# Performance work log

Hardware: AMD Instinct MI355X
Metric: run time of the kernel (lower is better)

Reference implementation:

```python
import jax, jax.numpy as jnp
import numpy as np

B, T, D, H = 16, 4096, 256, 512  # batch, seq_len, ninputs, nhiddens


def setup_inputs() -> dict:
    key = jax.random.key(0)
    k_x, k_ih, k_hh, k_b, k_bn = jax.random.split(key, 5)
    s = 1.0 / np.sqrt(H)
    xs = jax.random.normal(k_x, (B, T, D), dtype=jnp.float32)
    W_ih = jax.random.uniform(k_ih, (3 * H, D), minval=-s, maxval=s, dtype=jnp.float32)
    W_hh = jax.random.uniform(k_hh, (3 * H, H), minval=-s, maxval=s, dtype=jnp.float32)
    b = jax.random.uniform(k_b, (3 * H,), minval=-s, maxval=s, dtype=jnp.float32)
    b_n = jax.random.uniform(k_bn, (H,), minval=-s, maxval=s, dtype=jnp.float32)
    return {"xs": xs, "W_ih": W_ih, "W_hh": W_hh, "b": b, "b_n": b_n}


def _gru_scan(xs, W_ih, W_hh, b, b_n):
    # Precompute all input-side gates with one big GEMM: (B, T, 3H)
    igates = jnp.einsum('btd,gd->btg', xs, W_ih) + b

    def step(h, ig):
        # h: (B, H), ig: (B, 3H)
        hg = h @ W_hh.T  # (B, 3H)
        i_r, i_z, i_n = jnp.split(ig, 3, axis=-1)
        h_r, h_z, h_n = jnp.split(hg, 3, axis=-1)
        r = jax.nn.sigmoid(i_r + h_r)   # reset gate
        z = jax.nn.sigmoid(i_z + h_z)   # update gate (equinox 'inp')
        n = jnp.tanh(i_n + r * (h_n + b_n))
        h_new = n + z * (h - n)         # equinox: new + inp * (hidden - new)
        return h_new, h_new

    h0 = jnp.zeros((xs.shape[0], b_n.shape[0]), dtype=xs.dtype)
    _, ys = jax.lax.scan(step, h0, jnp.swapaxes(igates, 0, 1))  # (T, B, H)
    return jnp.swapaxes(ys, 0, 1)  # (B, T, H)


def reference(xs, W_ih, W_hh, b, b_n):
    # CellLayer('gru', 'deer') computes the exact GRU recurrence over time
    # (DEER's fixed point equals the sequential evaluation).
    return _gru_scan(xs, W_ih, W_hh, b, b_n)
```

## Files before the change

kernel.cpp:

```cpp
#include <hip/hip_runtime.h>
#include <stdint.h>
#include <stddef.h>

#define B_ 16
#define T_ 4096
#define D_ 256
#define H_ 512
#define G3_ 1536

#define OFF_IG   ((size_t)0)
#define OFF_WT   ((size_t)201326592)
#define OFF_MB   ((size_t)202899456)
#define WS_NEED  ((size_t)203423744)

#define PAR_STRIDE ((size_t)B_ * 8 * 512)

typedef _Float16 h2_t __attribute__((ext_vector_type(2)));

#if defined(__has_builtin)
#if __has_builtin(__builtin_amdgcn_fdot2)
#define HAVE_FDOT2 1
#endif
#endif

__device__ __forceinline__ float fdot2f(uint32_t w, uint32_t h, float acc) {
  union { uint32_t u; h2_t v; } a, b;
  a.u = w; b.u = h;
#ifdef HAVE_FDOT2
  return __builtin_amdgcn_fdot2(a.v, b.v, acc, false);
#else
  return fmaf((float)a.v.x, (float)b.v.x, fmaf((float)a.v.y, (float)b.v.y, acc));
#endif
}

__device__ __forceinline__ uint32_t packh2(float a, float b) {
  union { h2_t v; uint32_t u; } x;
  x.v.x = (_Float16)a; x.v.y = (_Float16)b;
  return x.u;
}

__device__ __forceinline__ uint32_t f16bits(float a) {
  union { _Float16 h; uint16_t u; } x;
  x.h = (_Float16)a;
  return (uint32_t)x.u;
}

__device__ __forceinline__ float h2f(uint16_t u) {
  union { _Float16 h; uint16_t u; } x;
  x.u = u;
  return (float)x.h;
}

__device__ __forceinline__ float sigmoidf_(float x) {
  return 1.0f / (1.0f + __expf(-x));
}

__device__ __forceinline__ float tanhf_(float x) {
  x = fminf(fmaxf(x, -15.0f), 15.0f);
  float e = __expf(-2.0f * x);
  return (1.0f - e) / (1.0f + e);
}

__global__ void __launch_bounds__(256) wt_kernel(const float* __restrict__ W, float4* __restrict__ Wt4) {
  int idx = blockIdx.x * 256 + threadIdx.x;
  if (idx >= G3_ * 64) return;
  int g = idx % G3_;
  int d4 = idx / G3_;
  float4 v = *(const float4*)(W + (size_t)g * D_ + 4 * d4);
  Wt4[(size_t)d4 * G3_ + g] = v;
}

__global__ void __launch_bounds__(256) ig_kernel(const float* __restrict__ xs,
                                                 const float* __restrict__ Wt,
                                                 const float* __restrict__ bias,
                                                 _Float16* __restrict__ ig) {
  __shared__ float xls[16 * 256];
  const int m0 = blockIdx.x * 16;
  const int tid = threadIdx.x;

  const float4* xsrc = (const float4*)(xs + (size_t)m0 * D_);
  float4* xdst = (float4*)xls;
#pragma unroll
  for (int k = 0; k < 4; ++k) xdst[tid + 256 * k] = xsrc[tid + 256 * k];
  __syncthreads();

  float acc[6][16];
#pragma unroll
  for (int k = 0; k < 6; ++k)
#pragma unroll
    for (int m = 0; m < 16; ++m) acc[k][m] = 0.0f;

  const float4* Wt4 = (const float4*)Wt;
  const float4* lds4 = (const float4*)xls;

  for (int d4 = 0; d4 < 64; ++d4) {
    float4 w[6];
#pragma unroll
    for (int k = 0; k < 6; ++k) w[k] = Wt4[(size_t)d4 * G3_ + tid + 256 * k];
#pragma unroll
    for (int m = 0; m < 16; ++m) {
      float4 xv = lds4[m * 64 + d4];
#pragma unroll
      for (int k = 0; k < 6; ++k) {
        acc[k][m] = fmaf(w[k].x, xv.x, acc[k][m]);
        acc[k][m] = fmaf(w[k].y, xv.y, acc[k][m]);
        acc[k][m] = fmaf(w[k].z, xv.z, acc[k][m]);
        acc[k][m] = fmaf(w[k].w, xv.w, acc[k][m]);
      }
    }
  }

#pragma unroll
  for (int k = 0; k < 6; ++k) {
    float bb = bias[tid + 256 * k];
#pragma unroll
    for (int m = 0; m < 16; ++m) {
      ig[(size_t)(m0 + m) * G3_ + tid + 256 * k] = (_Float16)(acc[k][m] + bb);
    }
  }
}

__global__ void __launch_bounds__(512, 1) rec_kernel(const _Float16* __restrict__ ig,
                                                     const float* __restrict__ Whh,
                                                     const float* __restrict__ bn,
                                                     uint32_t* __restrict__ mb,
                                                     float* __restrict__ out) {
  const int tid = threadIdx.x;
  const int wg = blockIdx.x;
  const int b = wg >> 3;
  const int s = wg & 7;
  const int q = tid & 7;
  const int c = tid >> 3;
  const int j = s * 64 + c;

  uint32_t wr[32], wz[32], wn[32];
  {
    const float4* s0 = (const float4*)(Whh + (size_t)j * H_ + q * 64);
    const float4* s1 = (const float4*)(Whh + (size_t)(j + H_) * H_ + q * 64);
    const float4* s2 = (const float4*)(Whh + (size_t)(j + 2 * H_) * H_ + q * 64);
#pragma unroll
    for (int i = 0; i < 16; ++i) {
      float4 v0 = s0[i]; wr[2 * i] = packh2(v0.x, v0.y); wr[2 * i + 1] = packh2(v0.z, v0.w);
      float4 v1 = s1[i]; wz[2 * i] = packh2(v1.x, v1.y); wz[2 * i + 1] = packh2(v1.z, v1.w);
      float4 v2 = s2[i]; wn[2 * i] = packh2(v2.x, v2.y); wn[2 * i + 1] = packh2(v2.z, v2.w);
    }
  }
  const float bnj = bn[j];

  __shared__ uint32_t hl[2][8][36];
  uint16_t* hl16 = (uint16_t*)hl;

  uint32_t* mypoll = mb + ((size_t)b * 8 + s) * 512 + tid;
  uint32_t* mypub  = mb + ((size_t)b * 8 + q) * 512 + j;

  const uint16_t* ig16 = (const uint16_t*)ig;
  size_t igbase = (size_t)b * T_ * G3_;

  uint16_t cr = ig16[igbase + j];
  uint16_t cz = ig16[igbase + j + H_];
  uint16_t cn = ig16[igbase + j + 2 * H_];
  uint16_t r1 = ig16[igbase + G3_ + j];
  uint16_t z1 = ig16[igbase + G3_ + j + H_];
  uint16_t n1 = ig16[igbase + G3_ + j + 2 * H_];
  uint16_t r2 = ig16[igbase + 2 * (size_t)G3_ + j];
  uint16_t z2 = ig16[igbase + 2 * (size_t)G3_ + j + H_];
  uint16_t n2 = ig16[igbase + 2 * (size_t)G3_ + j + 2 * H_];

  float hprev = 0.0f;

  for (int t = 0; t < T_; ++t) {
    uint16_t fr = 0, fz = 0, fn = 0;

    if (t > 0) {
      uint32_t* pb = mypoll + (size_t)(t & 1) * PAR_STRIDE;
      const uint32_t want = (uint32_t)t;
      uint32_t va, vb, a0 = 0;
      asm volatile("global_load_dword %0, %2, off sc1\n\t"
                   "global_load_dword %1, %2, off sc1"
                   : "=&v"(va), "=&v"(vb) : "v"(pb) : "memory");
      int it = 0;
      for (;;) {
        asm volatile("s_waitcnt vmcnt(1)" ::: "memory");
        __builtin_amdgcn_sched_barrier(0);
        a0 = va;
        if ((a0 >> 16) == want) break;
        asm volatile("global_load_dword %0, %1, off sc1" : "=&v"(va) : "v"(pb) : "memory");
        asm volatile("s_waitcnt vmcnt(1)" ::: "memory");
        __builtin_amdgcn_sched_barrier(0);
        a0 = vb;
        if ((a0 >> 16) == want) break;
        asm volatile("global_load_dword %0, %1, off sc1" : "=&v"(vb) : "v"(pb) : "memory");
        if (++it > (1 << 20)) { a0 = 0x7C00u; break; }
      }
      asm volatile("s_waitcnt vmcnt(0)" ::: "memory");
      __builtin_amdgcn_sched_barrier(0);

      hl16[(t & 1) * 576 + (tid >> 6) * 72 + (tid & 63)] = (uint16_t)(a0 & 0xFFFFu);
    }

    if (t + 3 < T_) {
      const size_t fb = igbase + 3 * (size_t)G3_;
      fr = ig16[fb + j];
      fz = ig16[fb + j + H_];
      fn = ig16[fb + j + 2 * H_];
    }

    __syncthreads();

    float ar = 0.0f, az = 0.0f, an = 0.0f;
    if (t > 0) {
      const uint4* hq = (const uint4*)hl[t & 1][q];
      uint4 hv[8];
#pragma unroll
      for (int i = 0; i < 8; ++i) hv[i] = hq[i];
      float ar0 = 0.0f, az0 = 0.0f, an0 = 0.0f;
      float ar1 = 0.0f, az1 = 0.0f, an1 = 0.0f;
#pragma unroll
      for (int i = 0; i < 4; ++i) {
        ar0 = fdot2f(wr[4 * i + 0], hv[i].x, ar0); az0 = fdot2f(wz[4 * i + 0], hv[i].x, az0); an0 = fdot2f(wn[4 * i + 0], hv[i].x, an0);
        ar0 = fdot2f(wr[4 * i + 1], hv[i].y, ar0); az0 = fdot2f(wz[4 * i + 1], hv[i].y, az0); an0 = fdot2f(wn[4 * i + 1], hv[i].y, an0);
        ar0 = fdot2f(wr[4 * i + 2], hv[i].z, ar0); az0 = fdot2f(wz[4 * i + 2], hv[i].z, az0); an0 = fdot2f(wn[4 * i + 2], hv[i].z, an0);
        ar0 = fdot2f(wr[4 * i + 3], hv[i].w, ar0); az0 = fdot2f(wz[4 * i + 3], hv[i].w, az0); an0 = fdot2f(wn[4 * i + 3], hv[i].w, an0);
      }
#pragma unroll
      for (int i = 4; i < 8; ++i) {
        ar1 = fdot2f(wr[4 * i + 0], hv[i].x, ar1); az1 = fdot2f(wz[4 * i + 0], hv[i].x, az1); an1 = fdot2f(wn[4 * i + 0], hv[i].x, an1);
        ar1 = fdot2f(wr[4 * i + 1], hv[i].y, ar1); az1 = fdot2f(wz[4 * i + 1], hv[i].y, az1); an1 = fdot2f(wn[4 * i + 1], hv[i].y, an1);
        ar1 = fdot2f(wr[4 * i + 2], hv[i].z, ar1); az1 = fdot2f(wz[4 * i + 2], hv[i].z, az1); an1 = fdot2f(wn[4 * i + 2], hv[i].z, an1);
        ar1 = fdot2f(wr[4 * i + 3], hv[i].w, ar1); az1 = fdot2f(wz[4 * i + 3], hv[i].w, az1); an1 = fdot2f(wn[4 * i + 3], hv[i].w, an1);
      }
      ar = ar0 + ar1; az = az0 + az1; an = an0 + an1;
      ar += __shfl_xor(ar, 1); ar += __shfl_xor(ar, 2); ar += __shfl_xor(ar, 4);
      az += __shfl_xor(az, 1); az += __shfl_xor(az, 2); az += __shfl_xor(az, 4);
      an += __shfl_xor(an, 1); an += __shfl_xor(an, 2); an += __shfl_xor(an, 4);
    }

    const float igr = h2f(cr), igz = h2f(cz), ign = h2f(cn);
    const float r = sigmoidf_(igr + ar);
    const float z = sigmoidf_(igz + az);
    const float n = tanhf_(ign + r * (an + bnj));
    const float hnew = n + z * (hprev - n);
    hprev = hnew;

    const uint32_t wv = ((uint32_t)(t + 1) << 16) | f16bits(hnew);
    __hip_atomic_store(mypub + (size_t)((t + 1) & 1) * PAR_STRIDE, wv,
                       __ATOMIC_RELAXED, __HIP_MEMORY_SCOPE_AGENT);
    if (q == 0) {
      out[((size_t)b * T_ + t) * H_ + j] = hnew;
    }
    asm volatile("s_waitcnt vmcnt(0)" ::: "memory");
    __builtin_amdgcn_sched_barrier(0);

    cr = r1; cz = z1; cn = n1;
    r1 = r2; z1 = z2; n1 = n2;
    r2 = fr; z2 = fz; n2 = fn;
    igbase += G3_;
  }
}

__global__ void __launch_bounds__(512) naive_kernel(const float* __restrict__ xs,
                                                    const float* __restrict__ Wih,
                                                    const float* __restrict__ Whh,
                                                    const float* __restrict__ bias,
                                                    const float* __restrict__ bn,
                                                    float* __restrict__ out) {
  const int b = blockIdx.x;
  const int j = threadIdx.x;
  __shared__ float h[H_];
  __shared__ float xr[D_];
  h[j] = 0.0f;
  __syncthreads();
  for (int t = 0; t < T_; ++t) {
    if (j < D_) xr[j] = xs[((size_t)b * T_ + t) * D_ + j];
    __syncthreads();
    float a[2];
#pragma unroll
    for (int g = 0; g < 2; ++g) {
      const int row = j + g * H_;
      float ssum = bias[row];
      const float* wi = Wih + (size_t)row * D_;
      for (int d = 0; d < D_; ++d) ssum = fmaf(wi[d], xr[d], ssum);
      const float* wh = Whh + (size_t)row * H_;
      for (int kk = 0; kk < H_; ++kk) ssum = fmaf(wh[kk], h[kk], ssum);
      a[g] = ssum;
    }
    const float r = sigmoidf_(a[0]);
    const float z = sigmoidf_(a[1]);
    float i_n = bias[j + 2 * H_];
    {
      const float* wi = Wih + (size_t)(j + 2 * H_) * D_;
      for (int d = 0; d < D_; ++d) i_n = fmaf(wi[d], xr[d], i_n);
    }
    float h_n = 0.0f;
    {
      const float* wh = Whh + (size_t)(j + 2 * H_) * H_;
      for (int kk = 0; kk < H_; ++kk) h_n = fmaf(wh[kk], h[kk], h_n);
    }
    const float nn = tanhf_(i_n + r * (h_n + bn[j]));
    const float hnew = nn + z * (h[j] - nn);
    __syncthreads();
    h[j] = hnew;
    out[((size_t)b * T_ + t) * H_ + j] = hnew;
  }
}

extern "C" void kernel_launch(void* const* d_in, const int* in_sizes, int n_in,
                              void* d_out, int out_size, void* d_ws, size_t ws_size,
                              hipStream_t stream) {
  const float* xs  = (const float*)d_in[0];
  const float* Wih = (const float*)d_in[1];
  const float* Whh = (const float*)d_in[2];
  const float* bia = (const float*)d_in[3];
  const float* bnp = (const float*)d_in[4];
  float* out = (float*)d_out;

  if (ws_size >= WS_NEED) {
    char* ws = (char*)d_ws;
    _Float16* igp = (_Float16*)(ws + OFF_IG);
    float* wtp = (float*)(ws + OFF_WT);
    uint32_t* mbp = (uint32_t*)(ws + OFF_MB);

    hipMemsetAsync(mbp, 0, 2 * PAR_STRIDE * sizeof(uint32_t), stream);

    wt_kernel<<<dim3(384), dim3(256), 0, stream>>>(Wih, (float4*)wtp);
    ig_kernel<<<dim3((B_ * T_) / 16), dim3(256), 0, stream>>>(xs, wtp, bia, igp);
    rec_kernel<<<dim3(128), dim3(512), 0, stream>>>(igp, Whh, bnp, mbp, out);
  } else {
    naive_kernel<<<dim3(B_), dim3(H_), 0, stream>>>(xs, Wih, Whh, bia, bnp, out);
  }
}
```

Baseline: 7.269 ms.

## Interleave mailbox by hidden unit so pollers read all slice copies in one vector load

The inter-block mailbox layout changes from [batch][slice][unit] to [batch][unit][slice], so the eight published copies of each hidden value sit in 32 contiguous bytes. Each poller now issues two dwordx4 loads covering all eight copies and accepts whichever carries the current step tag, instead of polling only its own slice's copy. The aim is to cut spin latency in the recurrent synchronization, since any publisher that arrives first satisfies the wait. In exchange, each poll moves more bytes, and the outstanding loads are left in flight until the step's final waitcnt.

```diff
diff --git a/kernel.cpp b/kernel.cpp
--- a/kernel.cpp
+++ b/kernel.cpp
@@ -13,7 +13,7 @@
 #define OFF_MB   ((size_t)202899456)
 #define WS_NEED  ((size_t)203423744)
 
-#define PAR_STRIDE ((size_t)B_ * 8 * 512)
+#define PAR_STRIDE ((size_t)B_ * 512 * 8)
 
 typedef _Float16 h2_t __attribute__((ext_vector_type(2)));
 
@@ -150,8 +150,8 @@
   __shared__ uint32_t hl[2][8][36];
   uint16_t* hl16 = (uint16_t*)hl;
 
-  uint32_t* mypoll = mb + ((size_t)b * 8 + s) * 512 + tid;
-  uint32_t* mypub  = mb + ((size_t)b * 8 + q) * 512 + j;
+  uint32_t* mypoll = mb + ((size_t)b * 512 + tid) * 8;
+  uint32_t* mypub  = mb + ((size_t)b * 512 + j) * 8 + q;
 
   const uint16_t* ig16 = (const uint16_t*)ig;
   size_t igbase = (size_t)b * T_ * G3_;
@@ -170,30 +170,35 @@
 
   for (int t = 0; t < T_; ++t) {
     uint16_t fr = 0, fz = 0, fn = 0;
+    uint4 xa = {0, 0, 0, 0}, xb = {0, 0, 0, 0};
 
     if (t > 0) {
       uint32_t* pb = mypoll + (size_t)(t & 1) * PAR_STRIDE;
       const uint32_t want = (uint32_t)t;
-      uint32_t va, vb, a0 = 0;
-      asm volatile("global_load_dword %0, %2, off sc1\n\t"
-                   "global_load_dword %1, %2, off sc1"
-                   : "=&v"(va), "=&v"(vb) : "v"(pb) : "memory");
+      uint32_t a0 = 0;
+      asm volatile("global_load_dwordx4 %0, %2, off sc1\n\t"
+                   "global_load_dwordx4 %1, %2, off offset:16 sc1"
+                   : "=&v"(xa), "=&v"(xb) : "v"(pb) : "memory");
       int it = 0;
       for (;;) {
         asm volatile("s_waitcnt vmcnt(1)" ::: "memory");
         __builtin_amdgcn_sched_barrier(0);
-        a0 = va;
-        if ((a0 >> 16) == want) break;
-        asm volatile("global_load_dword %0, %1, off sc1" : "=&v"(va) : "v"(pb) : "memory");
+        {
+          bool m0 = (xa.x >> 16) == want, m1 = (xa.y >> 16) == want;
+          bool m2 = (xa.z >> 16) == want, m3 = (xa.w >> 16) == want;
+          if (m0 | m1 | m2 | m3) { a0 = m0 ? xa.x : m1 ? xa.y : m2 ? xa.z : xa.w; break; }
+        }
+        asm volatile("global_load_dwordx4 %0, %1, off sc1" : "=&v"(xa) : "v"(pb) : "memory");
         asm volatile("s_waitcnt vmcnt(1)" ::: "memory");
         __builtin_amdgcn_sched_barrier(0);
-        a0 = vb;
-        if ((a0 >> 16) == want) break;
-        asm volatile("global_load_dword %0, %1, off sc1" : "=&v"(vb) : "v"(pb) : "memory");
+        {
+          bool m0 = (xb.x >> 16) == want, m1 = (xb.y >> 16) == want;
+          bool m2 = (xb.z >> 16) == want, m3 = (xb.w >> 16) == want;
+          if (m0 | m1 | m2 | m3) { a0 = m0 ? xb.x : m1 ? xb.y : m2 ? xb.z : xb.w; break; }
+        }
+        asm volatile("global_load_dwordx4 %0, %1, off offset:16 sc1" : "=&v"(xb) : "v"(pb) : "memory");
         if (++it > (1 << 20)) { a0 = 0x7C00u; break; }
       }
-      asm volatile("s_waitcnt vmcnt(0)" ::: "memory");
-      __builtin_amdgcn_sched_barrier(0);
 
       hl16[(t & 1) * 576 + (tid >> 6) * 72 + (tid & 63)] = (uint16_t)(a0 & 0xFFFFu);
     }
@@ -248,6 +253,8 @@
     if (q == 0) {
       out[((size_t)b * T_ + t) * H_ + j] = hnew;
     }
+    asm volatile("" :: "v"(xa.x), "v"(xa.y), "v"(xa.z), "v"(xa.w),
+                       "v"(xb.x), "v"(xb.y), "v"(xb.z), "v"(xb.w));
     asm volatile("s_waitcnt vmcnt(0)" ::: "memory");
     __builtin_amdgcn_sched_barrier(0);
 
@@ -320,7 +327,7 @@
     float* wtp = (float*)(ws + OFF_WT);
     uint32_t* mbp = (uint32_t*)(ws + OFF_MB);
 
-    hipMemsetAsync(mbp, 0, 2 * PAR_STRIDE * sizeof(uint32_t), stream);
+    (void)hipMemsetAsync(mbp, 0, 2 * PAR_STRIDE * sizeof(uint32_t), stream);
 
     wt_kernel<<<dim3(384), dim3(256), 0, stream>>>(Wih, (float4*)wtp);
     ig_kernel<<<dim3((B_ * T_) / 16), dim3(256), 0, stream>>>(xs, wtp, bia, igp);
```

After: 8.933 ms. 1.23x slower.

## Process two batch elements per recurrent workgroup, halving grid size

Applied to the files above, without the earlier changes.

Each recurrent workgroup now handles two batch rows (b and b+8) with the same register-resident W_hh slice, polling both mailboxes and computing both matvecs per step. The grid shrinks from 128 to 64 workgroups, so the cross-workgroup synchronization footprint shrinks and the loaded weights serve twice the work. The cost is a longer serial per-step critical path, since two polls and two matvecs run back-to-back inside each timestep.

```diff
diff --git a/kernel.cpp b/kernel.cpp
--- a/kernel.cpp
+++ b/kernel.cpp
@@ -127,7 +127,8 @@
                                                      float* __restrict__ out) {
   const int tid = threadIdx.x;
   const int wg = blockIdx.x;
-  const int b = wg >> 3;
+  const int b0 = wg >> 3;
+  const int b1 = b0 + 8;
   const int s = wg & 7;
   const int q = tid & 7;
   const int c = tid >> 3;
@@ -147,114 +148,179 @@
   }
   const float bnj = bn[j];
 
-  __shared__ uint32_t hl[2][8][36];
+  __shared__ uint32_t hl[2][2][8][36];
   uint16_t* hl16 = (uint16_t*)hl;
 
-  uint32_t* mypoll = mb + ((size_t)b * 8 + s) * 512 + tid;
-  uint32_t* mypub  = mb + ((size_t)b * 8 + q) * 512 + j;
+  uint32_t* poll0 = mb + ((size_t)b0 * 8 + s) * 512 + tid;
+  uint32_t* poll1 = mb + ((size_t)b1 * 8 + s) * 512 + tid;
+  uint32_t* pub0  = mb + ((size_t)b0 * 8 + q) * 512 + j;
+  uint32_t* pub1  = mb + ((size_t)b1 * 8 + q) * 512 + j;
 
   const uint16_t* ig16 = (const uint16_t*)ig;
-  size_t igbase = (size_t)b * T_ * G3_;
-
-  uint16_t cr = ig16[igbase + j];
-  uint16_t cz = ig16[igbase + j + H_];
-  uint16_t cn = ig16[igbase + j + 2 * H_];
-  uint16_t r1 = ig16[igbase + G3_ + j];
-  uint16_t z1 = ig16[igbase + G3_ + j + H_];
-  uint16_t n1 = ig16[igbase + G3_ + j + 2 * H_];
-  uint16_t r2 = ig16[igbase + 2 * (size_t)G3_ + j];
-  uint16_t z2 = ig16[igbase + 2 * (size_t)G3_ + j + H_];
-  uint16_t n2 = ig16[igbase + 2 * (size_t)G3_ + j + 2 * H_];
-
-  float hprev = 0.0f;
+  size_t igb0 = (size_t)b0 * T_ * G3_;
+  size_t igb1 = (size_t)b1 * T_ * G3_;
+
+  uint16_t cr0 = ig16[igb0 + j], cz0 = ig16[igb0 + j + H_], cn0 = ig16[igb0 + j + 2 * H_];
+  uint16_t r10 = ig16[igb0 + G3_ + j], z10 = ig16[igb0 + G3_ + j + H_], n10 = ig16[igb0 + G3_ + j + 2 * H_];
+  uint16_t r20 = ig16[igb0 + 2 * (size_t)G3_ + j], z20 = ig16[igb0 + 2 * (size_t)G3_ + j + H_], n20 = ig16[igb0 + 2 * (size_t)G3_ + j + 2 * H_];
+  uint16_t cr1 = ig16[igb1 + j], cz1 = ig16[igb1 + j + H_], cn1 = ig16[igb1 + j + 2 * H_];
+  uint16_t r11_ = ig16[igb1 + G3_ + j], z11 = ig16[igb1 + G3_ + j + H_], n11 = ig16[igb1 + G3_ + j + 2 * H_];
+  uint16_t r21 = ig16[igb1 + 2 * (size_t)G3_ + j], z21 = ig16[igb1 + 2 * (size_t)G3_ + j + H_], n21 = ig16[igb1 + 2 * (size_t)G3_ + j + 2 * H_];
+
+  float hprev0 = 0.0f, hprev1 = 0.0f;
 
   for (int t = 0; t < T_; ++t) {
-    uint16_t fr = 0, fz = 0, fn = 0;
+    uint16_t fr0 = 0, fz0 = 0, fn0 = 0, fr1 = 0, fz1 = 0, fn1 = 0;
 
     if (t > 0) {
-      uint32_t* pb = mypoll + (size_t)(t & 1) * PAR_STRIDE;
       const uint32_t want = (uint32_t)t;
-      uint32_t va, vb, a0 = 0;
-      asm volatile("global_load_dword %0, %2, off sc1\n\t"
-                   "global_load_dword %1, %2, off sc1"
-                   : "=&v"(va), "=&v"(vb) : "v"(pb) : "memory");
-      int it = 0;
-      for (;;) {
-        asm volatile("s_waitcnt vmcnt(1)" ::: "memory");
+      const size_t poff = (size_t)(t & 1) * PAR_STRIDE;
+
+      {
+        uint32_t* pb = poll0 + poff;
+        uint32_t va, vb, a0;
+        asm volatile("global_load_dword %0, %2, off sc1\n\t"
+                     "global_load_dword %1, %2, off sc1"
+                     : "=&v"(va), "=&v"(vb) : "v"(pb) : "memory");
+        int it = 0;
+        for (;;) {
+          asm volatile("s_waitcnt vmcnt(1)" ::: "memory");
+          __builtin_amdgcn_sched_barrier(0);
+          a0 = va;
+          if ((a0 >> 16) == want) break;
+          asm volatile("global_load_dword %0, %1, off sc1" : "=&v"(va) : "v"(pb) : "memory");
+          asm volatile("s_waitcnt vmcnt(1)" ::: "memory");
+          __builtin_amdgcn_sched_barrier(0);
+          a0 = vb;
+          if ((a0 >> 16) == want) break;
+          asm volatile("global_load_dword %0, %1, off sc1" : "=&v"(vb) : "v"(pb) : "memory");
+          if (++it > (1 << 20)) { a0 = 0x7C00u; break; }
+        }
+        asm volatile("s_waitcnt vmcnt(0)" :: "v"(va), "v"(vb) : "memory");
         __builtin_amdgcn_sched_barrier(0);
-        a0 = va;
-        if ((a0 >> 16) == want) break;
-        asm volatile("global_load_dword %0, %1, off sc1" : "=&v"(va) : "v"(pb) : "memory");
-        asm volatile("s_waitcnt vmcnt(1)" ::: "memory");
+        hl16[(t & 1) * 576 + (tid >> 6) * 72 + (tid & 63)] = (uint16_t)(a0 & 0xFFFFu);
+      }
+
+      {
+        uint32_t* pb = poll1 + poff;
+        uint32_t va, vb, a1;
+        asm volatile("global_load_dword %0, %2, off sc1\n\t"
+                     "global_load_dword %1, %2, off sc1"
+                     : "=&v"(va), "=&v"(vb) : "v"(pb) : "memory");
+        int it = 0;
+        for (;;) {
+          asm volatile("s_waitcnt vmcnt(1)" ::: "memory");
+          __builtin_amdgcn_sched_barrier(0);
+          a1 = va;
+          if ((a1 >> 16) == want) break;
+          asm volatile("global_load_dword %0, %1, off sc1" : "=&v"(va) : "v"(pb) : "memory");
+          asm volatile("s_waitcnt vmcnt(1)" ::: "memory");
+          __builtin_amdgcn_sched_barrier(0);
+          a1 = vb;
+          if ((a1 >> 16) == want) break;
+          asm volatile("global_load_dword %0, %1, off sc1" : "=&v"(vb) : "v"(pb) : "memory");
+          if (++it > (1 << 20)) { a1 = 0x7C00u; break; }
+        }
+        asm volatile("s_waitcnt vmcnt(0)" :: "v"(va), "v"(vb) : "memory");
         __builtin_amdgcn_sched_barrier(0);
-        a0 = vb;
-        if ((a0 >> 16) == want) break;
-        asm volatile("global_load_dword %0, %1, off sc1" : "=&v"(vb) : "v"(pb) : "memory");
-        if (++it > (1 << 20)) { a0 = 0x7C00u; break; }
-      }
-      asm volatile("s_waitcnt vmcnt(0)" ::: "memory");
-      __builtin_amdgcn_sched_barrier(0);
-
-      hl16[(t & 1) * 576 + (tid >> 6) * 72 + (tid & 63)] = (uint16_t)(a0 & 0xFFFFu);
-    }
+        hl16[1152 + (t & 1) * 576 + (tid >> 6) * 72 + (tid & 63)] = (uint16_t)(a1 & 0xFFFFu);
+      }
+    }
+
+    __syncthreads();
 
     if (t + 3 < T_) {
-      const size_t fb = igbase + 3 * (size_t)G3_;
-      fr = ig16[fb + j];
-      fz = ig16[fb + j + H_];
-      fn = ig16[fb + j + 2 * H_];
-    }
-
-    __syncthreads();
-
-    float ar = 0.0f, az = 0.0f, an = 0.0f;
-    if (t > 0) {
-      const uint4* hq = (const uint4*)hl[t & 1][q];
-      uint4 hv[8];
-#pragma unroll
-      for (int i = 0; i < 8; ++i) hv[i] = hq[i];
-      float ar0 = 0.0f, az0 = 0.0f, an0 = 0.0f;
-      float ar1 = 0.0f, az1 = 0.0f, an1 = 0.0f;
-#pragma unroll
-      for (int i = 0; i < 4; ++i) {
-        ar0 = fdot2f(wr[4 * i + 0], hv[i].x, ar0); az0 = fdot2f(wz[4 * i + 0], hv[i].x, az0); an0 = fdot2f(wn[4 * i + 0], hv[i].x, an0);
-        ar0 = fdot2f(wr[4 * i + 1], hv[i].y, ar0); az0 = fdot2f(wz[4 * i + 1], hv[i].y, az0); an0 = fdot2f(wn[4 * i + 1], hv[i].y, an0);
-        ar0 = fdot2f(wr[4 * i + 2], hv[i].z, ar0); az0 = fdot2f(wz[4 * i + 2], hv[i].z, az0); an0 = fdot2f(wn[4 * i + 2], hv[i].z, an0);
-        ar0 = fdot2f(wr[4 * i + 3], hv[i].w, ar0); az0 = fdot2f(wz[4 * i + 3], hv[i].w, az0); an0 = fdot2f(wn[4 * i + 3], hv[i].w, an0);
-      }
-#pragma unroll
-      for (int i = 4; i < 8; ++i) {
-        ar1 = fdot2f(wr[4 * i + 0], hv[i].x, ar1); az1 = fdot2f(wz[4 * i + 0], hv[i].x, az1); an1 = fdot2f(wn[4 * i + 0], hv[i].x, an1);
-        ar1 = fdot2f(wr[4 * i + 1], hv[i].y, ar1); az1 = fdot2f(wz[4 * i + 1], hv[i].y, az1); an1 = fdot2f(wn[4 * i + 1], hv[i].y, an1);
-        ar1 = fdot2f(wr[4 * i + 2], hv[i].z, ar1); az1 = fdot2f(wz[4 * i + 2], hv[i].z, az1); an1 = fdot2f(wn[4 * i + 2], hv[i].z, an1);
-        ar1 = fdot2f(wr[4 * i + 3], hv[i].w, ar1); az1 = fdot2f(wz[4 * i + 3], hv[i].w, az1); an1 = fdot2f(wn[4 * i + 3], hv[i].w, an1);
-      }
-      ar = ar0 + ar1; az = az0 + az1; an = an0 + an1;
-      ar += __shfl_xor(ar, 1); ar += __shfl_xor(ar, 2); ar += __shfl_xor(ar, 4);
-      az += __shfl_xor(az, 1); az += __shfl_xor(az, 2); az += __shfl_xor(az, 4);
-      an += __shfl_xor(an, 1); an += __shfl_xor(an, 2); an += __shfl_xor(an, 4);
-    }
-
-    const float igr = h2f(cr), igz = h2f(cz), ign = h2f(cn);
-    const float r = sigmoidf_(igr + ar);
-    const float z = sigmoidf_(igz + az);
-    const float n = tanhf_(ign + r * (an + bnj));
-    const float hnew = n + z * (hprev - n);
-    hprev = hnew;
-
-    const uint32_t wv = ((uint32_t)(t + 1) << 16) | f16bits(hnew);
-    __hip_atomic_store(mypub + (size_t)((t + 1) & 1) * PAR_STRIDE, wv,
-                       __ATOMIC_RELAXED, __HIP_MEMORY_SCOPE_AGENT);
-    if (q == 0) {
-      out[((size_t)b * T_ + t) * H_ + j] = hnew;
-    }
+      const size_t fb0 = igb0 + 3 * (size_t)G3_;
+      const size_t fb1 = igb1 + 3 * (size_t)G3_;
+      fr0 = ig16[fb0 + j]; fz0 = ig16[fb0 + j + H_]; fn0 = ig16[fb0 + j + 2 * H_];
+      fr1 = ig16[fb1 + j]; fz1 = ig16[fb1 + j + H_]; fn1 = ig16[fb1 + j + 2 * H_];
+    }
+
+    {
+      float ar = 0.0f, az = 0.0f, an = 0.0f;
+      if (t > 0) {
+        const uint4* hq = (const uint4*)hl[0][t & 1][q];
+        uint4 hv[8];
+#pragma unroll
+        for (int i = 0; i < 8; ++i) hv[i] = hq[i];
+        float ar0 = 0.0f, az0 = 0.0f, an0 = 0.0f, ar1 = 0.0f, az1 = 0.0f, an1 = 0.0f;
+#pragma unroll
+        for (int i = 0; i < 4; ++i) {
+          ar0 = fdot2f(wr[4 * i + 0], hv[i].x, ar0); az0 = fdot2f(wz[4 * i + 0], hv[i].x, az0); an0 = fdot2f(wn[4 * i + 0], hv[i].x, an0);
+          ar0 = fdot2f(wr[4 * i + 1], hv[i].y, ar0); az0 = fdot2f(wz[4 * i + 1], hv[i].y, az0); an0 = fdot2f(wn[4 * i + 1], hv[i].y, an0);
+          ar0 = fdot2f(wr[4 * i + 2], hv[i].z, ar0); az0 = fdot2f(wz[4 * i + 2], hv[i].z, az0); an0 = fdot2f(wn[4 * i + 2], hv[i].z, an0);
+          ar0 = fdot2f(wr[4 * i + 3], hv[i].w, ar0); az0 = fdot2f(wz[4 * i + 3], hv[i].w, az0); an0 = fdot2f(wn[4 * i + 3], hv[i].w, an0);
+        }
+#pragma unroll
+        for (int i = 4; i < 8; ++i) {
+          ar1 = fdot2f(wr[4 * i + 0], hv[i].x, ar1); az1 = fdot2f(wz[4 * i + 0], hv[i].x, az1); an1 = fdot2f(wn[4 * i + 0], hv[i].x, an1);
+          ar1 = fdot2f(wr[4 * i + 1], hv[i].y, ar1); az1 = fdot2f(wz[4 * i + 1], hv[i].y, az1); an1 = fdot2f(wn[4 * i + 1], hv[i].y, an1);
+          ar1 = fdot2f(wr[4 * i + 2], hv[i].z, ar1); az1 = fdot2f(wz[4 * i + 2], hv[i].z, az1); an1 = fdot2f(wn[4 * i + 2], hv[i].z, an1);
+          ar1 = fdot2f(wr[4 * i + 3], hv[i].w, ar1); az1 = fdot2f(wz[4 * i + 3], hv[i].w, az1); an1 = fdot2f(wn[4 * i + 3], hv[i].w, an1);
+        }
+        ar = ar0 + ar1; az = az0 + az1; an = an0 + an1;
+        ar += __shfl_xor(ar, 1); ar += __shfl_xor(ar, 2); ar += __shfl_xor(ar, 4);
+        az += __shfl_xor(az, 1); az += __shfl_xor(az, 2); az += __shfl_xor(az, 4);
+        an += __shfl_xor(an, 1); an += __shfl_xor(an, 2); an += __shfl_xor(an, 4);
+      }
+      const float igr = h2f(cr0), igz = h2f(cz0), ign = h2f(cn0);
+      const float r = sigmoidf_(igr + ar);
+      const float z = sigmoidf_(igz + az);
+      const float n = tanhf_(ign + r * (an + bnj));
+      const float hnew = n + z * (hprev0 - n);
+      hprev0 = hnew;
+      const uint32_t wv = ((uint32_t)(t + 1) << 16) | f16bits(hnew);
+      __hip_atomic_store(pub0 + (size_t)((t + 1) & 1) * PAR_STRIDE, wv,
+                         __ATOMIC_RELAXED, __HIP_MEMORY_SCOPE_AGENT);
+      if (q == 0) out[((size_t)b0 * T_ + t) * H_ + j] = hnew;
+    }
+
+    {
+      float ar = 0.0f, az = 0.0f, an = 0.0f;
+      if (t > 0) {
+        const uint4* hq = (const uint4*)hl[1][t & 1][q];
+        uint4 hv[8];
+#pragma unroll
+        for (int i = 0; i < 8; ++i) hv[i] = hq[i];
+        float ar0 = 0.0f, az0 = 0.0f, an0 = 0.0f, ar1 = 0.0f, az1 = 0.0f, an1 = 0.0f;
+#pragma unroll
+        for (int i = 0; i < 4; ++i) {
+          ar0 = fdot2f(wr[4 * i + 0], hv[i].x, ar0); az0 = fdot2f(wz[4 * i + 0], hv[i].x, az0); an0 = fdot2f(wn[4 * i + 0], hv[i].x, an0);
+          ar0 = fdot2f(wr[4 * i + 1], hv[i].y, ar0); az0 = fdot2f(wz[4 * i + 1], hv[i].y, az0); an0 = fdot2f(wn[4 * i + 1], hv[i].y, an0);
+          ar0 = fdot2f(wr[4 * i + 2], hv[i].z, ar0); az0 = fdot2f(wz[4 * i + 2], hv[i].z, az0); an0 = fdot2f(wn[4 * i + 2], hv[i].z, an0);
+          ar0 = fdot2f(wr[4 * i + 3], hv[i].w, ar0); az0 = fdot2f(wz[4 * i + 3], hv[i].w, az0); an0 = fdot2f(wn[4 * i + 3], hv[i].w, an0);
+        }
+#pragma unroll
+        for (int i = 4; i < 8; ++i) {
+          ar1 = fdot2f(wr[4 * i + 0], hv[i].x, ar1); az1 = fdot2f(wz[4 * i + 0], hv[i].x, az1); an1 = fdot2f(wn[4 * i + 0], hv[i].x, an1);
+          ar1 = fdot2f(wr[4 * i + 1], hv[i].y, ar1); az1 = fdot2f(wz[4 * i + 1], hv[i].y, az1); an1 = fdot2f(wn[4 * i + 1], hv[i].y, an1);
+          ar1 = fdot2f(wr[4 * i + 2], hv[i].z, ar1); az1 = fdot2f(wz[4 * i + 2], hv[i].z, az1); an1 = fdot2f(wn[4 * i + 2], hv[i].z, an1);
+          ar1 = fdot2f(wr[4 * i + 3], hv[i].w, ar1); az1 = fdot2f(wz[4 * i + 3], hv[i].w, az1); an1 = fdot2f(wn[4 * i + 3], hv[i].w, an1);
+        }
+        ar = ar0 + ar1; az = az0 + az1; an = an0 + an1;
+        ar += __shfl_xor(ar, 1); ar += __shfl_xor(ar, 2); ar += __shfl_xor(ar, 4);
+        az += __shfl_xor(az, 1); az += __shfl_xor(az, 2); az += __shfl_xor(az, 4);
+        an += __shfl_xor(an, 1); an += __shfl_xor(an, 2); an += __shfl_xor(an, 4);
+      }
+      const float igr = h2f(cr1), igz = h2f(cz1), ign = h2f(cn1);
+      const float r = sigmoidf_(igr + ar);
+      const float z = sigmoidf_(igz + az);
+      const float n = tanhf_(ign + r * (an + bnj));
+      const float hnew = n + z * (hprev1 - n);
+      hprev1 = hnew;
+      const uint32_t wv = ((uint32_t)(t + 1) << 16) | f16bits(hnew);
+      __hip_atomic_store(pub1 + (size_t)((t + 1) & 1) * PAR_STRIDE, wv,
+                         __ATOMIC_RELAXED, __HIP_MEMORY_SCOPE_AGENT);
+      if (q == 0) out[((size_t)b1 * T_ + t) * H_ + j] = hnew;
+    }
+
     asm volatile("s_waitcnt vmcnt(0)" ::: "memory");
     __builtin_amdgcn_sched_barrier(0);
 
-    cr = r1; cz = z1; cn = n1;
-    r1 = r2; z1 = z2; n1 = n2;
-    r2 = fr; z2 = fz; n2 = fn;
-    igbase += G3_;
+    cr0 = r10; cz0 = z10; cn0 = n10;  r10 = r20; z10 = z20; n10 = n20;  r20 = fr0; z20 = fz0; n20 = fn0;
+    cr1 = r11_; cz1 = z11; cn1 = n11; r11_ = r21; z11 = z21; n11 = n21; r21 = fr1; z21 = fz1; n21 = fn1;
+    igb0 += G3_;
+    igb1 += G3_;
   }
 }
 
@@ -320,11 +386,11 @@
     float* wtp = (float*)(ws + OFF_WT);
     uint32_t* mbp = (uint32_t*)(ws + OFF_MB);
 
-    hipMemsetAsync(mbp, 0, 2 * PAR_STRIDE * sizeof(uint32_t), stream);
+    (void)hipMemsetAsync(mbp, 0, 2 * PAR_STRIDE * sizeof(uint32_t), stream);
 
     wt_kernel<<<dim3(384), dim3(256), 0, stream>>>(Wih, (float4*)wtp);
     ig_kernel<<<dim3((B_ * T_) / 16), dim3(256), 0, stream>>>(xs, wtp, bia, igp);
-    rec_kernel<<<dim3(128), dim3(512), 0, stream>>>(igp, Whh, bnp, mbp, out);
+    rec_kernel<<<dim3(64), dim3(512), 0, stream>>>(igp, Whh, bnp, mbp, out);
   } else {
     naive_kernel<<<dim3(B_), dim3(H_), 0, stream>>>(xs, Wih, Whh, bia, bnp, out);
   }
```

Measured after the change: 11.83 ms. 1.63x slower.
